# Kernel tuning notes

Hardware: AMD Instinct MI355X
Metric: run time of the kernel (lower is better)

Reference implementation:

```python
import jax, jax.numpy as jnp
import numpy as np

HEADS = 4
DIM_HEAD = 32
EPS = 1e-5


def setup_inputs() -> dict:
    key = jax.random.key(0)
    ks = jax.random.split(key, 3)
    b, c, h, w = 32, 128, 128, 128
    hidden = HEADS * DIM_HEAD  # 128
    x = jax.random.normal(ks[0], (b, c, h, w), dtype=jnp.float32)
    Wqkv = jax.random.normal(ks[1], (3 * hidden, c), dtype=jnp.float32) * (1.0 / np.sqrt(c))
    Wout = jax.random.normal(ks[2], (c, hidden), dtype=jnp.float32) * (1.0 / np.sqrt(hidden))
    bout = jnp.zeros((c,), dtype=jnp.float32)
    g = jnp.ones((c,), dtype=jnp.float32)
    return {"x": x, "Wqkv": Wqkv, "Wout": Wout, "bout": bout, "g": g}


def reference(x, Wqkv, Wout, bout, g):
    b, c, h, w = x.shape
    n = h * w
    scale = DIM_HEAD ** -0.5
    # 1x1 conv (no bias) == channel GEMM
    qkv = jnp.einsum('oc,bchw->bohw', Wqkv, x)  # [b, 3*hidden, h, w]
    q, k, v = jnp.split(qkv, 3, axis=1)
    # b (h d) x y -> b h d n
    def to_heads(t):
        return t.reshape(b, HEADS, DIM_HEAD, n)
    q, k, v = to_heads(q), to_heads(k), to_heads(v)
    q = jax.nn.softmax(q, axis=-2) * scale   # softmax over per-head channel dim
    k = jax.nn.softmax(k, axis=-1)           # softmax over token dim
    v = v / n
    ctx = jnp.einsum('bhdn,bhen->bhde', k, v)   # [b, heads, d, e]
    out = jnp.einsum('bhde,bhdn->bhen', ctx, q)  # [b, heads, e, n]
    out = out.reshape(b, HEADS * DIM_HEAD, h, w)
    # output 1x1 conv with bias
    y = jnp.einsum('oc,bchw->bohw', Wout, out) + bout[None, :, None, None]
    # LayerNorm over channel dim (biased variance)
    mean = jnp.mean(y, axis=1, keepdims=True)
    var = jnp.var(y, axis=1, keepdims=True)
    return (y - mean) * jax.lax.rsqrt(var + EPS) * g[None, :, None, None]
```

## Files before the change

kernel.cpp:

```cpp
#include <hip/hip_runtime.h>
#include <math.h>


#define NCHUNK 64

typedef __attribute__((ext_vector_type(8))) short short8;
typedef __attribute__((ext_vector_type(4))) float f32x4;

__device__ __forceinline__ uint bf16r(float f) {
    uint u = __float_as_uint(f);
    return (u + 0x7FFFu + ((u >> 16) & 1u)) >> 16;
}
__device__ __forceinline__ float bf16f(uint h) { return __uint_as_float(h << 16); }
__device__ __forceinline__ uint2 bsplit(float f) {
    uint h = bf16r(f);
    float r = f - bf16f(h);
    return make_uint2(h, bf16r(r));
}
__device__ __forceinline__ uint2 bsplit_t(float f) {
    uint u = __float_as_uint(f);
    uint uh = u & 0xFFFF0000u;
    float r = f - __uint_as_float(uh);
    return make_uint2(uh >> 16, __float_as_uint(r) >> 16);
}
__device__ __forceinline__ uint bpack_t(float f) {
    uint u = __float_as_uint(f);
    uint uh = u & 0xFFFF0000u;
    float r = f - __uint_as_float(uh);
    return (uh >> 16) | (__float_as_uint(r) & 0xFFFF0000u);
}
__device__ __forceinline__ short8 lo8(uint4 a, uint4 b) {
    uint4 r;
    r.x = (a.x & 0xFFFFu) | (a.y << 16);
    r.y = (a.z & 0xFFFFu) | (a.w << 16);
    r.z = (b.x & 0xFFFFu) | (b.y << 16);
    r.w = (b.z & 0xFFFFu) | (b.w << 16);
    return __builtin_bit_cast(short8, r);
}
__device__ __forceinline__ short8 hi8(uint4 a, uint4 b) {
    uint4 r;
    r.x = (a.x >> 16) | (a.y & 0xFFFF0000u);
    r.y = (a.z >> 16) | (a.w & 0xFFFF0000u);
    r.z = (b.x >> 16) | (b.y & 0xFFFF0000u);
    r.w = (b.z >> 16) | (b.w & 0xFFFF0000u);
    return __builtin_bit_cast(short8, r);
}

__global__ __launch_bounds__(256)
void wsplit(const float* __restrict__ W, ushort* __restrict__ Wh,
            ushort* __restrict__ Wl, int n)
{
    const int base = (blockIdx.x * 256 + threadIdx.x) * 4;
    if (base + 3 < n) {
        const float4 f = *(const float4*)(W + base);
        const uint2 a = bsplit(f.x), b2 = bsplit(f.y), c = bsplit(f.z), d = bsplit(f.w);
        ushort4 hh; hh.x = (ushort)a.x; hh.y = (ushort)b2.x; hh.z = (ushort)c.x; hh.w = (ushort)d.x;
        ushort4 ll; ll.x = (ushort)a.y; ll.y = (ushort)b2.y; ll.z = (ushort)c.y; ll.w = (ushort)d.y;
        *(ushort4*)(Wh + base) = hh;
        *(ushort4*)(Wl + base) = ll;
    }
}

#define MFMA(A, B, C) __builtin_amdgcn_mfma_f32_16x16x32_bf16((A), (B), (C), 0, 0, 0)

__global__ __launch_bounds__(512, 1)
void la_k1(const float* __restrict__ x,
           const ushort* __restrict__ Wh, const ushort* __restrict__ Wl,
           float* __restrict__ Spart, float* __restrict__ Zpart)
{
    __shared__ __align__(16) char smb[163840];

    const int tid = threadIdx.x;
    const int b = blockIdx.y, chunk = blockIdx.x;
    const int w = tid >> 6, l = tid & 63;
    const int l15 = l & 15, lg = l >> 4;

    {
#pragma unroll
        for (int it = 0; it < 16; ++it) {
            const int q = tid + 512 * it;
            const int region = q >> 12;
            const int lin = (q & 4095) * 16;
            const int r = lin >> 8;
            const int dst = (region << 16) + (lin ^ ((r & 7) << 4));
            const ushort* src = (region ? Wl : Wh) + 128 * 128 + (lin >> 1);
            *(uint4*)(&smb[dst]) = *(const uint4*)src;
        }
    }

    f32x4 s2[2];
#pragma unroll
    for (int i = 0; i < 2; ++i) s2[i] = (f32x4){0.f, 0.f, 0.f, 0.f};
    float zrow[4];
#pragma unroll
    for (int i = 0; i < 4; ++i) zrow[i] = 0.f;

    const int hh = w >> 1, eh = w & 1;

    for (int t = 0; t < 8; ++t) {
        const int p0 = chunk * 256 + t * 32;
        {
            const float* xb = x + (size_t)b * 128 * 16384 + p0;
            const int cp = tid >> 3, j = tid & 7;
            const int pb = j * 4, c = cp * 2;
            const float4 a = *(const float4*)(xb + (size_t)c * 16384 + pb);
            const float4 bq = *(const float4*)(xb + (size_t)(c + 1) * 16384 + pb);
            const float av[4] = {a.x, a.y, a.z, a.w};
            const float bv[4] = {bq.x, bq.y, bq.z, bq.w};
#pragma unroll
            for (int pp = 0; pp < 4; ++pp) {
                const uint2 s0 = bsplit_t(av[pp]);
                const uint2 s1 = bsplit_t(bv[pp]);
                const int p = pb + pp;
                const int byt = (p * 256 + c * 2) ^ (((p ^ (p >> 3)) & 7) << 4);
                *(uint*)(&smb[131072 + byt])        = s0.x | (s1.x << 16);
                *(uint*)(&smb[131072 + 8192 + byt]) = s0.y | (s1.y << 16);
            }
        }
        __syncthreads();

        f32x4 acc[2][2];
#pragma unroll
        for (int rt = 0; rt < 2; ++rt)
#pragma unroll
            for (int ct = 0; ct < 2; ++ct) acc[rt][ct] = (f32x4){0.f, 0.f, 0.f, 0.f};
#pragma unroll
        for (int ks = 0; ks < 4; ++ks) {
            short8 Bh[2], Bl[2];
#pragma unroll
            for (int ct = 0; ct < 2; ++ct) {
                const int p = ct * 16 + l15;
                const int byt = (p * 256 + (ks * 32 + lg * 8) * 2) ^ (((p ^ (p >> 3)) & 7) << 4);
                Bh[ct] = *(const short8*)(&smb[131072 + byt]);
                Bl[ct] = *(const short8*)(&smb[131072 + 8192 + byt]);
            }
#pragma unroll
            for (int rt = 0; rt < 2; ++rt) {
                const int r = (w + rt * 8) * 16 + l15;
                const int abyt = (r * 256 + (ks * 32 + lg * 8) * 2) ^ ((r & 7) << 4);
                const short8 Ah_ = *(const short8*)(&smb[abyt]);
                const short8 Al_ = *(const short8*)(&smb[65536 + abyt]);
#pragma unroll
                for (int ct = 0; ct < 2; ++ct) {
                    acc[rt][ct] = MFMA(Ah_, Bh[ct], acc[rt][ct]);
                    acc[rt][ct] = MFMA(Ah_, Bl[ct], acc[rt][ct]);
                    acc[rt][ct] = MFMA(Al_, Bh[ct], acc[rt][ct]);
                }
            }
        }
        __syncthreads();

#pragma unroll
        for (int rt = 0; rt < 2; ++rt) {
            const bool isk = (rt == 0);
#pragma unroll
            for (int ct = 0; ct < 2; ++ct) {
                const int p = ct * 16 + l15;
#pragma unroll
                for (int i = 0; i < 4; ++i) {
                    float val = acc[rt][ct][i];
                    if (isk) {
                        val = expf(val);
                        zrow[i] += val;
                    }
                    const int r = w * 16 + lg * 4 + i;
                    const int byt = (r * 128 + p * 4) ^ ((r & 7) << 4);
                    *(uint*)(&smb[131072 + (isk ? 0 : 16384) + byt]) = bpack_t(val);
                }
            }
        }
        __syncthreads();

        {
            short8 A2h[2], A2l[2], B2h, B2l;
#pragma unroll
            for (int rt2 = 0; rt2 < 2; ++rt2) {
                const int r = hh * 32 + rt2 * 16 + l15;
                const int b0 = (r * 128 + lg * 32) ^ ((r & 7) << 4);
                const int b1 = (r * 128 + lg * 32 + 16) ^ ((r & 7) << 4);
                const uint4 q0 = *(const uint4*)(&smb[131072 + b0]);
                const uint4 q1 = *(const uint4*)(&smb[131072 + b1]);
                A2h[rt2] = lo8(q0, q1);
                A2l[rt2] = hi8(q0, q1);
            }
            {
                const int rv = hh * 32 + eh * 16 + l15;
                const int c0 = (rv * 128 + lg * 32) ^ ((rv & 7) << 4);
                const int c1 = (rv * 128 + lg * 32 + 16) ^ ((rv & 7) << 4);
                const uint4 r0 = *(const uint4*)(&smb[131072 + 16384 + c0]);
                const uint4 r1 = *(const uint4*)(&smb[131072 + 16384 + c1]);
                B2h = lo8(r0, r1);
                B2l = hi8(r0, r1);
            }
#pragma unroll
            for (int rt2 = 0; rt2 < 2; ++rt2) {
                s2[rt2] = MFMA(A2h[rt2], B2h, s2[rt2]);
                s2[rt2] = MFMA(A2h[rt2], B2l, s2[rt2]);
                s2[rt2] = MFMA(A2l[rt2], B2h, s2[rt2]);
            }
        }
        __syncthreads();
    }

    const size_t sbase = (((size_t)b * NCHUNK + chunk) * 4 + hh) * 1024;
#pragma unroll
    for (int rt2 = 0; rt2 < 2; ++rt2)
#pragma unroll
        for (int i = 0; i < 4; ++i) {
            const int d = rt2 * 16 + lg * 4 + i;
            const int e = eh * 16 + l15;
            Spart[sbase + d * 32 + e] = s2[rt2][i];
        }

#pragma unroll
    for (int i = 0; i < 4; ++i) {
        float z = zrow[i];
        z += __shfl_xor(z, 1, 64);
        z += __shfl_xor(z, 2, 64);
        z += __shfl_xor(z, 4, 64);
        z += __shfl_xor(z, 8, 64);
        if (l15 == 0)
            Zpart[((size_t)b * NCHUNK + chunk) * 128 + w * 16 + lg * 4 + i] = z;
    }
}

__global__ __launch_bounds__(256, 1)
void la_k1_reduce(const float* __restrict__ Spart, const float* __restrict__ Zpart,
                  float* __restrict__ ctxF)
{
    const int tid = threadIdx.x;
    const int b  = blockIdx.x >> 2;
    const int hh = blockIdx.x & 3;
    const int d  = tid >> 3;
    const int e0 = (tid & 7) << 2;
    float sx = 0.f, sy = 0.f, sz = 0.f, sw = 0.f, z = 0.f;
    for (int ch = 0; ch < NCHUNK; ++ch) {
        const size_t base = (((size_t)b * NCHUNK + ch) * 4 + hh) * 32 + d;
        const float4 v = *(const float4*)(Spart + base * 32 + e0);
        sx += v.x; sy += v.y; sz += v.z; sw += v.w;
        z += Zpart[base];
    }
    const float inv = 1.0f / (z * 16384.0f);
    float4 r; r.x = sx * inv; r.y = sy * inv; r.z = sz * inv; r.w = sw * inv;
    *(float4*)(ctxF + ((((size_t)b * 4 + hh) * 32 + d) << 5) + e0) = r;
}

__global__ __launch_bounds__(256, 1)
void la_mk(const float* __restrict__ Wout, const float* __restrict__ ctxF,
           ushort* __restrict__ Mh, ushort* __restrict__ Ml)
{
    __shared__ float ctxs[4096];
    const int b = blockIdx.x;
    const int tid = threadIdx.x;
#pragma unroll
    for (int i = 0; i < 4; ++i) {
        const int idx = (tid + 256 * i) * 4;
        *(float4*)(ctxs + idx) = *(const float4*)(ctxF + (size_t)b * 4096 + idx);
    }
    __syncthreads();
    const int cp = tid & 127;
    const int dh = tid >> 7;
#pragma unroll
    for (int hq = 0; hq < 2; ++hq) {
        const int h = dh * 2 + hq;
        float wrow[32];
#pragma unroll
        for (int e4 = 0; e4 < 8; ++e4) {
            const float4 wv = *(const float4*)(Wout + cp * 128 + h * 32 + e4 * 4);
            wrow[e4 * 4 + 0] = wv.x; wrow[e4 * 4 + 1] = wv.y;
            wrow[e4 * 4 + 2] = wv.z; wrow[e4 * 4 + 3] = wv.w;
        }
        for (int d = 0; d < 32; ++d) {
            float m = 0.f;
#pragma unroll
            for (int e = 0; e < 32; ++e)
                m += wrow[e] * ctxs[h * 1024 + d * 32 + e];
            const uint2 s = bsplit(m);
            const size_t mo = (size_t)b * 16384 + cp * 128 + h * 32 + d;
            Mh[mo] = (ushort)s.x;
            Ml[mo] = (ushort)s.y;
        }
    }
}

__device__ __forceinline__ int xswz64(int p, int cbyte) {
    return (p * 256 + cbyte) ^ (((p ^ (p >> 3)) & 7) << 4);
}
__device__ __forceinline__ int qswz(int p, int off) {
    return (p * 64 + off) ^ (((p >> 1) & 3) << 4);
}

__global__ __launch_bounds__(512, 1)
void la_k2s(const float* __restrict__ x,
            const ushort* __restrict__ Wqh, const ushort* __restrict__ Wql,
            const ushort* __restrict__ Mh, const ushort* __restrict__ Ml,
            const float* __restrict__ bout, const float* __restrict__ g,
            float* __restrict__ outg)
{
    __shared__ __align__(16) char smb[163840];

    const int tid = threadIdx.x;
    const int b = blockIdx.y, blk = blockIdx.x;
    const int w = tid >> 6, l = tid & 63;
    const int l15 = l & 15, lg = l >> 4;
    const int hq = w >> 1, ph = w & 1;

    {
        const ushort* mhb = Mh + (size_t)b * 16384;
        const ushort* mlb = Ml + (size_t)b * 16384;
#pragma unroll
        for (int it = 0; it < 16; ++it) {
            const int q = tid + 512 * it;
            const int plane = q >> 11;
            const int lin = (q & 2047) * 16;
            const int r = lin >> 8;
            const int dst = plane * 32768 + (lin ^ ((r & 7) << 4));
            const ushort* src = (plane == 0 ? Wqh : plane == 1 ? Wql
                               : plane == 2 ? mhb : mlb) + (lin >> 1);
            *(uint4*)(&smb[dst]) = *(const uint4*)src;
        }
    }

    const float4 bo = *(const float4*)(bout + w * 16 + lg * 4);
    const float4 gv = *(const float4*)(g + w * 16 + lg * 4);

    for (int it = 0; it < 32; ++it) {
        const int p0 = blk * 2048 + it * 64;

        {
            const float* xb = x + (size_t)b * 128 * 16384 + p0;
            const int j = tid & 15, gq = tid >> 4;
            const int pb = j * 4, cb = gq * 4;
            const float4 xv0 = *(const float4*)(xb + (size_t)(cb + 0) * 16384 + pb);
            const float4 xv1 = *(const float4*)(xb + (size_t)(cb + 1) * 16384 + pb);
            const float4 xv2 = *(const float4*)(xb + (size_t)(cb + 2) * 16384 + pb);
            const float4 xv3 = *(const float4*)(xb + (size_t)(cb + 3) * 16384 + pb);
            float rc[4][4];
            rc[0][0] = xv0.x; rc[0][1] = xv0.y; rc[0][2] = xv0.z; rc[0][3] = xv0.w;
            rc[1][0] = xv1.x; rc[1][1] = xv1.y; rc[1][2] = xv1.z; rc[1][3] = xv1.w;
            rc[2][0] = xv2.x; rc[2][1] = xv2.y; rc[2][2] = xv2.z; rc[2][3] = xv2.w;
            rc[3][0] = xv3.x; rc[3][1] = xv3.y; rc[3][2] = xv3.z; rc[3][3] = xv3.w;
#pragma unroll
            for (int pp = 0; pp < 4; ++pp) {
                const uint2 s0 = bsplit_t(rc[0][pp]);
                const uint2 s1 = bsplit_t(rc[1][pp]);
                const uint2 s2u = bsplit_t(rc[2][pp]);
                const uint2 s3 = bsplit_t(rc[3][pp]);
                const int p = pb + pp;
                const int byt = xswz64(p, cb * 2);
                *(uint2*)(&smb[131072 + byt]) = make_uint2(s0.x | (s1.x << 16), s2u.x | (s3.x << 16));
                *(uint2*)(&smb[147456 + byt]) = make_uint2(s0.y | (s1.y << 16), s2u.y | (s3.y << 16));
            }
        }
        __syncthreads();

        f32x4 qacc[2][2];
#pragma unroll
        for (int t_ = 0; t_ < 2; ++t_)
#pragma unroll
            for (int ct = 0; ct < 2; ++ct) qacc[t_][ct] = (f32x4){0.f, 0.f, 0.f, 0.f};
#pragma unroll
        for (int ks = 0; ks < 4; ++ks) {
            short8 Bh[2], Bl[2];
#pragma unroll
            for (int ct = 0; ct < 2; ++ct) {
                const int p = ph * 32 + ct * 16 + l15;
                const int byt = xswz64(p, (ks * 32 + lg * 8) * 2);
                Bh[ct] = *(const short8*)(&smb[131072 + byt]);
                Bl[ct] = *(const short8*)(&smb[147456 + byt]);
            }
#pragma unroll
            for (int t_ = 0; t_ < 2; ++t_) {
                const int r = hq * 32 + t_ * 16 + l15;
                const int abyt = (r * 256 + (ks * 32 + lg * 8) * 2) ^ ((r & 7) << 4);
                const short8 Ah_ = *(const short8*)(&smb[abyt]);
                const short8 Al_ = *(const short8*)(&smb[32768 + abyt]);
#pragma unroll
                for (int ct = 0; ct < 2; ++ct) {
                    qacc[t_][ct] = MFMA(Ah_, Bh[ct], qacc[t_][ct]);
                    qacc[t_][ct] = MFMA(Ah_, Bl[ct], qacc[t_][ct]);
                    qacc[t_][ct] = MFMA(Al_, Bh[ct], qacc[t_][ct]);
                }
            }
        }

        float vv[2][2][4];
#pragma unroll
        for (int ct = 0; ct < 2; ++ct) {
            float s = 0.f;
#pragma unroll
            for (int t_ = 0; t_ < 2; ++t_)
#pragma unroll
                for (int i = 0; i < 4; ++i) {
                    vv[ct][t_][i] = expf(qacc[t_][ct][i]);
                    s += vv[ct][t_][i];
                }
            s += __shfl_xor(s, 16, 64);
            s += __shfl_xor(s, 32, 64);
            const float inv = 0.17677669529663687f / s;
#pragma unroll
            for (int t_ = 0; t_ < 2; ++t_)
#pragma unroll
                for (int i = 0; i < 4; ++i) vv[ct][t_][i] *= inv;
        }
        __syncthreads();

#pragma unroll
        for (int ct = 0; ct < 2; ++ct) {
            const int p = ph * 32 + ct * 16 + l15;
#pragma unroll
            for (int t_ = 0; t_ < 2; ++t_) {
                const uint2 a0 = bsplit_t(vv[ct][t_][0]);
                const uint2 a1 = bsplit_t(vv[ct][t_][1]);
                const uint2 a2 = bsplit_t(vv[ct][t_][2]);
                const uint2 a3 = bsplit_t(vv[ct][t_][3]);
                const int byt = hq * 4096 + qswz(p, (t_ * 16 + lg * 4) * 2);
                *(uint2*)(&smb[131072 + byt]) = make_uint2(a0.x | (a1.x << 16), a2.x | (a3.x << 16));
                *(uint2*)(&smb[147456 + byt]) = make_uint2(a0.y | (a1.y << 16), a2.y | (a3.y << 16));
            }
        }
        __syncthreads();

        f32x4 yacc[4];
#pragma unroll
        for (int ct = 0; ct < 4; ++ct) yacc[ct] = (f32x4){0.f, 0.f, 0.f, 0.f};
#pragma unroll
        for (int ks = 0; ks < 4; ++ks) {
            const int r = w * 16 + l15;
            const int abyt = (r * 256 + (ks * 32 + lg * 8) * 2) ^ ((r & 7) << 4);
            const short8 Ah_ = *(const short8*)(&smb[65536 + abyt]);
            const short8 Al_ = *(const short8*)(&smb[98304 + abyt]);
#pragma unroll
            for (int ct = 0; ct < 4; ++ct) {
                const int p = ct * 16 + l15;
                const int byt = ks * 4096 + qswz(p, lg * 16);
                const short8 Bh_ = *(const short8*)(&smb[131072 + byt]);
                const short8 Bl_ = *(const short8*)(&smb[147456 + byt]);
                yacc[ct] = MFMA(Ah_, Bh_, yacc[ct]);
                yacc[ct] = MFMA(Ah_, Bl_, yacc[ct]);
                yacc[ct] = MFMA(Al_, Bh_, yacc[ct]);
            }
        }
        __syncthreads();

#pragma unroll
        for (int ct = 0; ct < 4; ++ct) {
            yacc[ct][0] += bo.x; yacc[ct][1] += bo.y;
            yacc[ct][2] += bo.z; yacc[ct][3] += bo.w;
        }
        float* lnred = (float*)(smb + 131072);
#pragma unroll
        for (int ct = 0; ct < 4; ++ct) {
            float s = 0.f, q = 0.f;
#pragma unroll
            for (int i = 0; i < 4; ++i) {
                const float yv = yacc[ct][i];
                s += yv; q += yv * yv;
            }
            s += __shfl_xor(s, 16, 64); q += __shfl_xor(q, 16, 64);
            s += __shfl_xor(s, 32, 64); q += __shfl_xor(q, 32, 64);
            if (lg == 0) {
                const int p = ct * 16 + l15;
                lnred[(p * 8 + w) * 2 + 0] = s;
                lnred[(p * 8 + w) * 2 + 1] = q;
            }
        }
        __syncthreads();
#pragma unroll
        for (int ct = 0; ct < 4; ++ct) {
            const int p = ct * 16 + l15;
            float st = 0.f, qt = 0.f;
#pragma unroll
            for (int ww = 0; ww < 8; ++ww) {
                st += lnred[(p * 8 + ww) * 2 + 0];
                qt += lnred[(p * 8 + ww) * 2 + 1];
            }
            const float mean = st * (1.0f / 128.0f);
            const float var  = qt * (1.0f / 128.0f) - mean * mean;
            const float rstd = 1.0f / sqrtf(var + 1e-5f);
            const float gg[4] = {gv.x, gv.y, gv.z, gv.w};
#pragma unroll
            for (int i = 0; i < 4; ++i) {
                const int o = w * 16 + lg * 4 + i;
                outg[((size_t)b * 128 + o) * 16384 + p0 + p] =
                    (yacc[ct][i] - mean) * rstd * gg[i];
            }
        }
        __syncthreads();
    }
}

extern "C" void kernel_launch(void* const* d_in, const int* in_sizes, int n_in,
                              void* d_out, int out_size, void* d_ws, size_t ws_size,
                              hipStream_t stream) {
    const float* x    = (const float*)d_in[0];
    const float* Wqkv = (const float*)d_in[1];
    const float* Wout = (const float*)d_in[2];
    const float* bout = (const float*)d_in[3];
    const float* g    = (const float*)d_in[4];
    float* out = (float*)d_out;

    float* Spart = (float*)d_ws;
    float* Zpart = Spart + (size_t)32 * NCHUNK * 4 * 32 * 32;
    float* ctxF  = Zpart + (size_t)32 * NCHUNK * 4 * 32;
    ushort* Wqh  = (ushort*)(ctxF + (size_t)32 * 4096);
    ushort* Wql  = Wqh + 384 * 128;
    ushort* Mh   = (ushort*)Spart;
    ushort* Ml   = Mh + (size_t)32 * 16384;
    (void)in_sizes; (void)n_in; (void)out_size; (void)ws_size;

    wsplit<<<dim3(48), 256, 0, stream>>>(Wqkv, Wqh, Wql, 384 * 128);
    la_k1<<<dim3(NCHUNK, 32), 512, 0, stream>>>(x, Wqh, Wql, Spart, Zpart);
    la_k1_reduce<<<dim3(128), 256, 0, stream>>>(Spart, Zpart, ctxF);
    la_mk<<<dim3(32), 256, 0, stream>>>(Wout, ctxF, Mh, Ml);
    la_k2s<<<dim3(8, 32), 512, 0, stream>>>(x, Wqh, Wql, Mh, Ml, bout, g, out);
}
```

Before: 452.7 us.

## Double waves per block in fused attention-output kernel to 1024 threads

Restructures the main fused kernel to use 16 waves instead of 8 per block, splitting the q-projection by head and 16-token tiles and the output GEMM by 16-channel tile and 32-token half. Each wave does half the MFMA work per iteration, and the x staging loads two channels per thread instead of four. This is meant to raise latency hiding on each CU given one block per CU due to LDS. In exchange, per-wave operand reuse drops and barrier costs span more waves.

```diff
diff --git a/kernel.cpp b/kernel.cpp
--- a/kernel.cpp
+++ b/kernel.cpp
@@ -290,8 +290,8 @@
     return (p * 64 + off) ^ (((p >> 1) & 3) << 4);
 }
 
-__global__ __launch_bounds__(512, 1)
-void la_k2s(const float* __restrict__ x,
+__global__ __launch_bounds__(1024, 1)
+void la_k2t(const float* __restrict__ x,
             const ushort* __restrict__ Wqh, const ushort* __restrict__ Wql,
             const ushort* __restrict__ Mh, const ushort* __restrict__ Ml,
             const float* __restrict__ bout, const float* __restrict__ g,
@@ -303,14 +303,15 @@
     const int b = blockIdx.y, blk = blockIdx.x;
     const int w = tid >> 6, l = tid & 63;
     const int l15 = l & 15, lg = l >> 4;
-    const int hq = w >> 1, ph = w & 1;
+    const int hq = w >> 2, pq = w & 3;
+    const int ot = w >> 1, ph2 = w & 1;
 
     {
         const ushort* mhb = Mh + (size_t)b * 16384;
         const ushort* mlb = Ml + (size_t)b * 16384;
 #pragma unroll
-        for (int it = 0; it < 16; ++it) {
-            const int q = tid + 512 * it;
+        for (int it = 0; it < 8; ++it) {
+            const int q = tid + 1024 * it;
             const int plane = q >> 11;
             const int lin = (q & 2047) * 16;
             const int r = lin >> 8;
@@ -321,79 +322,62 @@
         }
     }
 
-    const float4 bo = *(const float4*)(bout + w * 16 + lg * 4);
-    const float4 gv = *(const float4*)(g + w * 16 + lg * 4);
+    const float4 bo = *(const float4*)(bout + ot * 16 + lg * 4);
+    const float4 gv = *(const float4*)(g + ot * 16 + lg * 4);
 
     for (int it = 0; it < 32; ++it) {
         const int p0 = blk * 2048 + it * 64;
 
         {
             const float* xb = x + (size_t)b * 128 * 16384 + p0;
-            const int j = tid & 15, gq = tid >> 4;
-            const int pb = j * 4, cb = gq * 4;
-            const float4 xv0 = *(const float4*)(xb + (size_t)(cb + 0) * 16384 + pb);
-            const float4 xv1 = *(const float4*)(xb + (size_t)(cb + 1) * 16384 + pb);
-            const float4 xv2 = *(const float4*)(xb + (size_t)(cb + 2) * 16384 + pb);
-            const float4 xv3 = *(const float4*)(xb + (size_t)(cb + 3) * 16384 + pb);
-            float rc[4][4];
-            rc[0][0] = xv0.x; rc[0][1] = xv0.y; rc[0][2] = xv0.z; rc[0][3] = xv0.w;
-            rc[1][0] = xv1.x; rc[1][1] = xv1.y; rc[1][2] = xv1.z; rc[1][3] = xv1.w;
-            rc[2][0] = xv2.x; rc[2][1] = xv2.y; rc[2][2] = xv2.z; rc[2][3] = xv2.w;
-            rc[3][0] = xv3.x; rc[3][1] = xv3.y; rc[3][2] = xv3.z; rc[3][3] = xv3.w;
+            const int j = tid & 15, cq = tid >> 4;
+            const int pb = j * 4, c = cq * 2;
+            const float4 a = *(const float4*)(xb + (size_t)c * 16384 + pb);
+            const float4 bq = *(const float4*)(xb + (size_t)(c + 1) * 16384 + pb);
+            const float av[4] = {a.x, a.y, a.z, a.w};
+            const float bv[4] = {bq.x, bq.y, bq.z, bq.w};
 #pragma unroll
             for (int pp = 0; pp < 4; ++pp) {
-                const uint2 s0 = bsplit_t(rc[0][pp]);
-                const uint2 s1 = bsplit_t(rc[1][pp]);
-                const uint2 s2u = bsplit_t(rc[2][pp]);
-                const uint2 s3 = bsplit_t(rc[3][pp]);
+                const uint2 s0 = bsplit_t(av[pp]);
+                const uint2 s1 = bsplit_t(bv[pp]);
                 const int p = pb + pp;
-                const int byt = xswz64(p, cb * 2);
-                *(uint2*)(&smb[131072 + byt]) = make_uint2(s0.x | (s1.x << 16), s2u.x | (s3.x << 16));
-                *(uint2*)(&smb[147456 + byt]) = make_uint2(s0.y | (s1.y << 16), s2u.y | (s3.y << 16));
-            }
-        }
-        __syncthreads();
-
-        f32x4 qacc[2][2];
-#pragma unroll
-        for (int t_ = 0; t_ < 2; ++t_)
-#pragma unroll
-            for (int ct = 0; ct < 2; ++ct) qacc[t_][ct] = (f32x4){0.f, 0.f, 0.f, 0.f};
+                const int byt = xswz64(p, c * 2);
+                *(uint*)(&smb[131072 + byt]) = s0.x | (s1.x << 16);
+                *(uint*)(&smb[147456 + byt]) = s0.y | (s1.y << 16);
+            }
+        }
+        __syncthreads();
+
+        f32x4 qacc[2];
+        qacc[0] = (f32x4){0.f, 0.f, 0.f, 0.f};
+        qacc[1] = (f32x4){0.f, 0.f, 0.f, 0.f};
+        const int pQ = pq * 16 + l15;
 #pragma unroll
         for (int ks = 0; ks < 4; ++ks) {
-            short8 Bh[2], Bl[2];
-#pragma unroll
-            for (int ct = 0; ct < 2; ++ct) {
-                const int p = ph * 32 + ct * 16 + l15;
-                const int byt = xswz64(p, (ks * 32 + lg * 8) * 2);
-                Bh[ct] = *(const short8*)(&smb[131072 + byt]);
-                Bl[ct] = *(const short8*)(&smb[147456 + byt]);
-            }
+            const int byt = xswz64(pQ, (ks * 32 + lg * 8) * 2);
+            const short8 Bh_ = *(const short8*)(&smb[131072 + byt]);
+            const short8 Bl_ = *(const short8*)(&smb[147456 + byt]);
 #pragma unroll
             for (int t_ = 0; t_ < 2; ++t_) {
                 const int r = hq * 32 + t_ * 16 + l15;
                 const int abyt = (r * 256 + (ks * 32 + lg * 8) * 2) ^ ((r & 7) << 4);
                 const short8 Ah_ = *(const short8*)(&smb[abyt]);
                 const short8 Al_ = *(const short8*)(&smb[32768 + abyt]);
-#pragma unroll
-                for (int ct = 0; ct < 2; ++ct) {
-                    qacc[t_][ct] = MFMA(Ah_, Bh[ct], qacc[t_][ct]);
-                    qacc[t_][ct] = MFMA(Ah_, Bl[ct], qacc[t_][ct]);
-                    qacc[t_][ct] = MFMA(Al_, Bh[ct], qacc[t_][ct]);
-                }
-            }
-        }
-
-        float vv[2][2][4];
-#pragma unroll
-        for (int ct = 0; ct < 2; ++ct) {
+                qacc[t_] = MFMA(Ah_, Bh_, qacc[t_]);
+                qacc[t_] = MFMA(Ah_, Bl_, qacc[t_]);
+                qacc[t_] = MFMA(Al_, Bh_, qacc[t_]);
+            }
+        }
+
+        float vv[2][4];
+        {
             float s = 0.f;
 #pragma unroll
             for (int t_ = 0; t_ < 2; ++t_)
 #pragma unroll
                 for (int i = 0; i < 4; ++i) {
-                    vv[ct][t_][i] = expf(qacc[t_][ct][i]);
-                    s += vv[ct][t_][i];
+                    vv[t_][i] = expf(qacc[t_][i]);
+                    s += vv[t_][i];
                 }
             s += __shfl_xor(s, 16, 64);
             s += __shfl_xor(s, 32, 64);
@@ -401,38 +385,34 @@
 #pragma unroll
             for (int t_ = 0; t_ < 2; ++t_)
 #pragma unroll
-                for (int i = 0; i < 4; ++i) vv[ct][t_][i] *= inv;
-        }
-        __syncthreads();
-
-#pragma unroll
-        for (int ct = 0; ct < 2; ++ct) {
-            const int p = ph * 32 + ct * 16 + l15;
-#pragma unroll
-            for (int t_ = 0; t_ < 2; ++t_) {
-                const uint2 a0 = bsplit_t(vv[ct][t_][0]);
-                const uint2 a1 = bsplit_t(vv[ct][t_][1]);
-                const uint2 a2 = bsplit_t(vv[ct][t_][2]);
-                const uint2 a3 = bsplit_t(vv[ct][t_][3]);
-                const int byt = hq * 4096 + qswz(p, (t_ * 16 + lg * 4) * 2);
-                *(uint2*)(&smb[131072 + byt]) = make_uint2(a0.x | (a1.x << 16), a2.x | (a3.x << 16));
-                *(uint2*)(&smb[147456 + byt]) = make_uint2(a0.y | (a1.y << 16), a2.y | (a3.y << 16));
-            }
-        }
-        __syncthreads();
-
-        f32x4 yacc[4];
-#pragma unroll
-        for (int ct = 0; ct < 4; ++ct) yacc[ct] = (f32x4){0.f, 0.f, 0.f, 0.f};
+                for (int i = 0; i < 4; ++i) vv[t_][i] *= inv;
+        }
+        __syncthreads();
+
+#pragma unroll
+        for (int t_ = 0; t_ < 2; ++t_) {
+            const uint2 a0 = bsplit_t(vv[t_][0]);
+            const uint2 a1 = bsplit_t(vv[t_][1]);
+            const uint2 a2 = bsplit_t(vv[t_][2]);
+            const uint2 a3 = bsplit_t(vv[t_][3]);
+            const int byt = hq * 4096 + qswz(pQ, (t_ * 16 + lg * 4) * 2);
+            *(uint2*)(&smb[131072 + byt]) = make_uint2(a0.x | (a1.x << 16), a2.x | (a3.x << 16));
+            *(uint2*)(&smb[147456 + byt]) = make_uint2(a0.y | (a1.y << 16), a2.y | (a3.y << 16));
+        }
+        __syncthreads();
+
+        f32x4 yacc[2];
+        yacc[0] = (f32x4){0.f, 0.f, 0.f, 0.f};
+        yacc[1] = (f32x4){0.f, 0.f, 0.f, 0.f};
 #pragma unroll
         for (int ks = 0; ks < 4; ++ks) {
-            const int r = w * 16 + l15;
+            const int r = ot * 16 + l15;
             const int abyt = (r * 256 + (ks * 32 + lg * 8) * 2) ^ ((r & 7) << 4);
             const short8 Ah_ = *(const short8*)(&smb[65536 + abyt]);
             const short8 Al_ = *(const short8*)(&smb[98304 + abyt]);
 #pragma unroll
-            for (int ct = 0; ct < 4; ++ct) {
-                const int p = ct * 16 + l15;
+            for (int ct = 0; ct < 2; ++ct) {
+                const int p = ph2 * 32 + ct * 16 + l15;
                 const int byt = ks * 4096 + qswz(p, lg * 16);
                 const short8 Bh_ = *(const short8*)(&smb[131072 + byt]);
                 const short8 Bl_ = *(const short8*)(&smb[147456 + byt]);
@@ -444,13 +424,13 @@
         __syncthreads();
 
 #pragma unroll
-        for (int ct = 0; ct < 4; ++ct) {
+        for (int ct = 0; ct < 2; ++ct) {
             yacc[ct][0] += bo.x; yacc[ct][1] += bo.y;
             yacc[ct][2] += bo.z; yacc[ct][3] += bo.w;
         }
         float* lnred = (float*)(smb + 131072);
 #pragma unroll
-        for (int ct = 0; ct < 4; ++ct) {
+        for (int ct = 0; ct < 2; ++ct) {
             float s = 0.f, q = 0.f;
 #pragma unroll
             for (int i = 0; i < 4; ++i) {
@@ -460,15 +440,15 @@
             s += __shfl_xor(s, 16, 64); q += __shfl_xor(q, 16, 64);
             s += __shfl_xor(s, 32, 64); q += __shfl_xor(q, 32, 64);
             if (lg == 0) {
-                const int p = ct * 16 + l15;
-                lnred[(p * 8 + w) * 2 + 0] = s;
-                lnred[(p * 8 + w) * 2 + 1] = q;
-            }
-        }
-        __syncthreads();
-#pragma unroll
-        for (int ct = 0; ct < 4; ++ct) {
-            const int p = ct * 16 + l15;
+                const int p = ph2 * 32 + ct * 16 + l15;
+                lnred[(p * 8 + ot) * 2 + 0] = s;
+                lnred[(p * 8 + ot) * 2 + 1] = q;
+            }
+        }
+        __syncthreads();
+#pragma unroll
+        for (int ct = 0; ct < 2; ++ct) {
+            const int p = ph2 * 32 + ct * 16 + l15;
             float st = 0.f, qt = 0.f;
 #pragma unroll
             for (int ww = 0; ww < 8; ++ww) {
@@ -481,7 +461,7 @@
             const float gg[4] = {gv.x, gv.y, gv.z, gv.w};
 #pragma unroll
             for (int i = 0; i < 4; ++i) {
-                const int o = w * 16 + lg * 4 + i;
+                const int o = ot * 16 + lg * 4 + i;
                 outg[((size_t)b * 128 + o) * 16384 + p0 + p] =
                     (yacc[ct][i] - mean) * rstd * gg[i];
             }
@@ -513,5 +493,5 @@
     la_k1<<<dim3(NCHUNK, 32), 512, 0, stream>>>(x, Wqh, Wql, Spart, Zpart);
     la_k1_reduce<<<dim3(128), 256, 0, stream>>>(Spart, Zpart, ctxF);
     la_mk<<<dim3(32), 256, 0, stream>>>(Wout, ctxF, Mh, Ml);
-    la_k2s<<<dim3(8, 32), 512, 0, stream>>>(x, Wqh, Wql, Mh, Ml, bout, g, out);
-}
+    la_k2t<<<dim3(8, 32), 1024, 0, stream>>>(x, Wqh, Wql, Mh, Ml, bout, g, out);
+}
```

Measured after the change: 464.4 us. +2.6%, slower.
